# Kernel optimization log

Measured on AMD Instinct MI355X. Metric: run time of the kernel, lower is better.

The kernel has to match this reference:

```python
import jax, jax.numpy as jnp
import numpy as np

B, D_MODEL, HIDEEN, HEAD, IMG_H, IMG_W = 16, 512, 512, 8, 32, 32
D_K = D_MODEL // HEAD
EPS = 1e-5


def setup_inputs() -> dict:
    key = jax.random.key(0)
    ks = jax.random.split(key, 9)
    s_in = 1.0 / np.sqrt(D_MODEL)
    s_h = 1.0 / np.sqrt(HIDEEN)
    return {
        "x": jax.random.normal(ks[0], (B, D_MODEL, IMG_H, IMG_W), jnp.float32),
        "Wq": jax.random.uniform(ks[1], (HIDEEN, D_MODEL), jnp.float32, -s_in, s_in),
        "bq": jax.random.uniform(ks[2], (HIDEEN,), jnp.float32, -s_in, s_in),
        "Wk": jax.random.uniform(ks[3], (HIDEEN, D_MODEL), jnp.float32, -s_in, s_in),
        "bk": jax.random.uniform(ks[4], (HIDEEN,), jnp.float32, -s_in, s_in),
        "Wv": jax.random.uniform(ks[5], (HIDEEN, D_MODEL), jnp.float32, -s_in, s_in),
        "bv": jax.random.uniform(ks[6], (HIDEEN,), jnp.float32, -s_in, s_in),
        "Wo": jax.random.uniform(ks[7], (HIDEEN, HIDEEN), jnp.float32, -s_h, s_h),
        "bo": jax.random.uniform(ks[8], (HIDEEN,), jnp.float32, -s_h, s_h),
    }


def _conv1x1(x, W, b):
    # x: [B, Cin, H, W], W: [Cout, Cin]
    return jnp.einsum("bchw,oc->bohw", x, W) + b[None, :, None, None]


def _heads(t):
    # torch: [B, C, H, W] -> view(B, -1, head, d_k) -> transpose(1, 2)
    return t.reshape(B, -1, HEAD, D_K).transpose(0, 2, 1, 3)  # [B, head, N, d_k]


def reference(x, Wq, bq, Wk, bk, Wv, bv, Wo, bo):
    q = _heads(_conv1x1(x, Wq, bq))
    k = _heads(_conv1x1(x, Wk, bk))
    v = _heads(_conv1x1(x, Wv, bv))
    scores = jnp.einsum("bhnd,bhmd->bhnm", q, k) / np.sqrt(D_K).astype(np.float32)
    attn = jax.nn.softmax(scores, axis=-1)
    out = jnp.einsum("bhnm,bhmd->bhnd", attn, v)  # [B, head, N, d_k]
    # back to image layout: [B, N, head*d_k] -> [B, hideen, H, W]
    out = out.transpose(0, 2, 1, 3).reshape(B, -1, HEAD * D_K)
    out = out.transpose(0, 2, 1).reshape(B, -1, IMG_H, IMG_W)
    out = _conv1x1(out, Wo, bo)
    # InstanceNorm2d (affine=False, biased var, eps=1e-5)
    mu = out.mean(axis=(2, 3), keepdims=True)
    var = out.var(axis=(2, 3), keepdims=True)
    out = (out - mu) / jnp.sqrt(var + EPS)
    # original applies the SAME attn_out conv a second time
    out = _conv1x1(out, Wo, bo)
    return out
```

## Files before the change

### kernel.cpp

```cpp
#include <hip/hip_runtime.h>


typedef short bf16x8_t __attribute__((ext_vector_type(8)));
typedef float f32x4_t  __attribute__((ext_vector_type(4)));

union U4 { uint4 u; bf16x8_t v; unsigned short us[8]; };

__device__ __forceinline__ unsigned short f2bf(float f) {
  union { float f; unsigned int u; } x; x.f = f;
  unsigned int r = x.u + 0x7fffu + ((x.u >> 16) & 1u);
  return (unsigned short)(r >> 16);
}
__device__ __forceinline__ unsigned int f2bf2(float lo, float hi) {
  return (unsigned int)f2bf(lo) | ((unsigned int)f2bf(hi) << 16);
}
__device__ __forceinline__ void ld_lds16(const unsigned short* g,
                                         unsigned short* l) {
  __builtin_amdgcn_global_load_lds(
      (const __attribute__((address_space(1))) unsigned int*)g,
      (__attribute__((address_space(3))) unsigned int*)l, 16, 0, 0);
}

#define BATCH_STRIDE (512 * 1024)

__global__ __launch_bounds__(256) void cvtx_k(
    const float* __restrict__ x, unsigned short* __restrict__ xb)
{
  __shared__ float tile[32][33];
  const int b = blockIdx.z, c0 = blockIdx.y * 32, n0 = blockIdx.x * 32;
  const int t = threadIdx.x;
  {
    const int cr = t >> 3, n4 = (t & 7) * 4;
    const float4 u = *(const float4*)(x + (size_t)b * BATCH_STRIDE
                                      + (size_t)(c0 + cr) * 1024 + n0 + n4);
    tile[cr][n4] = u.x; tile[cr][n4 + 1] = u.y;
    tile[cr][n4 + 2] = u.z; tile[cr][n4 + 3] = u.w;
  }
  __syncthreads();
  {
    const int nl = t >> 3, c4 = (t & 7) * 4;
    uint2 o;
    o.x = f2bf2(tile[c4][nl], tile[c4 + 1][nl]);
    o.y = f2bf2(tile[c4 + 2][nl], tile[c4 + 3][nl]);
    *(uint2*)(xb + (size_t)b * BATCH_STRIDE + (size_t)(n0 + nl) * 512
              + c0 + c4) = o;
  }
}

template<int OUTF>
__device__ __forceinline__ void gemm_core(
    const float* __restrict__ W, const float* __restrict__ bias,
    const unsigned short* __restrict__ src, void* __restrict__ dst,
    int m0, int n0, int b, unsigned short* sA, unsigned short* sB)
{
  const int t = threadIdx.x;
  const int lane = t & 63, wv = t >> 6, qd = lane >> 4, cl = lane & 15;
  const int wm = wv >> 1, wn = wv & 1;
  const unsigned short* srcb = src + (size_t)b * BATCH_STRIDE + (size_t)n0 * 512;

  f32x4_t acc[4][4];
  #pragma unroll
  for (int i = 0; i < 4; ++i)
    #pragma unroll
    for (int f = 0; f < 4; ++f) acc[i][f] = (f32x4_t){0.f, 0.f, 0.f, 0.f};

  const int srow = t >> 2, sch = (t & 3) * 8;

  for (int kk = 0; kk < 512; kk += 32) {
    if (kk) __syncthreads();
    #pragma unroll
    for (int p = 0; p < 2; ++p) {
      ld_lds16(srcb + (size_t)(p * 64 + srow) * 512 + kk + sch,
               sB + p * 2048 + t * 8);
      const float* wr = W + (size_t)(m0 + p * 64 + srow) * 512 + kk + sch;
      const float4 w0 = *(const float4*)wr;
      const float4 w1 = *(const float4*)(wr + 4);
      uint4 wa;
      wa.x = f2bf2(w0.x, w0.y); wa.y = f2bf2(w0.z, w0.w);
      wa.z = f2bf2(w1.x, w1.y); wa.w = f2bf2(w1.z, w1.w);
      *(uint4*)(sA + p * 2048 + t * 8) = wa;
    }
    __syncthreads();
    U4 af[4], bfr[4];
    #pragma unroll
    for (int i = 0; i < 4; ++i) {
      af[i].u  = *(const uint4*)(sA + (wm * 64 + i * 16 + cl) * 32 + qd * 8);
      bfr[i].u = *(const uint4*)(sB + (wn * 64 + i * 16 + cl) * 32 + qd * 8);
    }
    #pragma unroll
    for (int i = 0; i < 4; ++i)
      #pragma unroll
      for (int f = 0; f < 4; ++f)
        acc[i][f] = __builtin_amdgcn_mfma_f32_16x16x32_bf16(
            af[i].v, bfr[f].v, acc[i][f], 0, 0, 0);
  }

  #pragma unroll
  for (int i = 0; i < 4; ++i) {
    #pragma unroll
    for (int r = 0; r < 4; ++r) {
      const int o = m0 + wm * 64 + i * 16 + qd * 4 + r;
      const float bv = bias[o];
      #pragma unroll
      for (int f = 0; f < 4; ++f) {
        const int n = n0 + wn * 64 + f * 16 + cl;
        const size_t idx = (size_t)b * BATCH_STRIDE + (size_t)o * 1024 + n;
        const float val = acc[i][f][r] + bv;
        if (OUTF) ((float*)dst)[idx] = val;
        else      ((unsigned short*)dst)[idx] = f2bf(val);
      }
    }
  }
}

struct QKVArgs {
  const float* W[3];
  const float* bias[3];
  unsigned short* dst[3];
};

__global__ __launch_bounds__(256) void qkv_k(
    QKVArgs args, const unsigned short* __restrict__ xb)
{
  __shared__ __align__(16) unsigned short sA[128 * 32];
  __shared__ __align__(16) unsigned short sB[128 * 32];
  const int widx = blockIdx.y >> 2;
  const int m0 = (blockIdx.y & 3) * 128;
  gemm_core<0>(args.W[widx], args.bias[widx], xb, args.dst[widx],
               m0, blockIdx.x * 128, blockIdx.z, sA, sB);
}

template<int OUTF>
__global__ __launch_bounds__(256) void gemm_wo_k(
    const float* __restrict__ W, const float* __restrict__ bias,
    const unsigned short* __restrict__ src, void* __restrict__ dst)
{
  __shared__ __align__(16) unsigned short sA[128 * 32];
  __shared__ __align__(16) unsigned short sB[128 * 32];
  gemm_core<OUTF>(W, bias, src, dst, blockIdx.y * 128, blockIdx.x * 128,
                  blockIdx.z, sA, sB);
}

__global__ __launch_bounds__(256) void vt_k(
    const unsigned short* __restrict__ V, unsigned short* __restrict__ Vt)
{
  __shared__ unsigned short sT[64 * 72];
  const int b = blockIdx.z, p0 = blockIdx.x * 64, j0 = blockIdx.y * 64;
  const int t = threadIdx.x;
  const int r = t >> 2, c8 = (t & 3) * 8;
  #pragma unroll
  for (int p = 0; p < 2; ++p)
    *(uint4*)(sT + r * 72 + c8 + p * 32) =
        *(const uint4*)(V + (size_t)b * BATCH_STRIDE
                        + (size_t)(p0 + r) * 512 + j0 + c8 + p * 32);
  __syncthreads();
  #pragma unroll
  for (int p = 0; p < 2; ++p) {
    U4 o;
    #pragma unroll
    for (int e = 0; e < 8; ++e) o.us[e] = sT[(c8 + p * 32 + e) * 72 + r];
    *(uint4*)(Vt + (size_t)b * BATCH_STRIDE + (size_t)(j0 + r) * 1024
              + p0 + c8 + p * 32) = o.u;
  }
}

__global__ __launch_bounds__(256) void attn_k(
    const unsigned short* __restrict__ Q,
    const unsigned short* __restrict__ K,
    const unsigned short* __restrict__ Vt,
    unsigned short* __restrict__ O)
{
  __shared__ __align__(16) unsigned short sK[64 * 80];
  __shared__ __align__(16) unsigned short sV[64 * 80];
  __shared__ __align__(16) unsigned short sP[4 * 32 * 80];

  const int t = threadIdx.x;
  const int lane = t & 63, wv = t >> 6, qd = lane >> 4, cl = lane & 15;
  const int b = blockIdx.y >> 3, h = blockIdx.y & 7;
  const int i0 = blockIdx.x * 128;
  const size_t bbase = (size_t)b * BATCH_STRIDE;
  const int hoff = h * 64;
  unsigned short* sPw = sP + wv * 2560;

  U4 aq[2][2];
  #pragma unroll
  for (int mt = 0; mt < 2; ++mt) {
    const unsigned short* qp =
        Q + bbase + (size_t)(i0 + wv * 32 + mt * 16 + cl) * 512 + hoff;
    aq[mt][0].u = *(const uint4*)(qp + qd * 8);
    aq[mt][1].u = *(const uint4*)(qp + 32 + qd * 8);
  }

  f32x4_t oacc[2][4];
  #pragma unroll
  for (int mt = 0; mt < 2; ++mt)
    #pragma unroll
    for (int f = 0; f < 4; ++f) oacc[mt][f] = (f32x4_t){0.f, 0.f, 0.f, 0.f};
  float rs[2][4] = {{0.f, 0.f, 0.f, 0.f}, {0.f, 0.f, 0.f, 0.f}};

  const int srow = t >> 2, sch = (t & 3) * 8;

  for (int j0 = 0; j0 < 1024; j0 += 64) {
    __syncthreads();
    #pragma unroll
    for (int p = 0; p < 2; ++p) {
      *(uint4*)(sK + srow * 80 + sch + p * 32) =
          *(const uint4*)(K + bbase + (size_t)(j0 + srow) * 512
                          + hoff + sch + p * 32);
      *(uint4*)(sV + srow * 80 + sch + p * 32) =
          *(const uint4*)(Vt + bbase + (size_t)(hoff + srow) * 1024
                          + j0 + sch + p * 32);
    }
    __syncthreads();

    f32x4_t s[2][4];
    #pragma unroll
    for (int nh = 0; nh < 4; ++nh) {
      U4 bk0, bk1;
      bk0.u = *(const uint4*)(sK + (nh * 16 + cl) * 80 + qd * 8);
      bk1.u = *(const uint4*)(sK + (nh * 16 + cl) * 80 + 32 + qd * 8);
      #pragma unroll
      for (int mt = 0; mt < 2; ++mt) {
        s[mt][nh] = (f32x4_t){0.f, 0.f, 0.f, 0.f};
        s[mt][nh] = __builtin_amdgcn_mfma_f32_16x16x32_bf16(
            aq[mt][0].v, bk0.v, s[mt][nh], 0, 0, 0);
        s[mt][nh] = __builtin_amdgcn_mfma_f32_16x16x32_bf16(
            aq[mt][1].v, bk1.v, s[mt][nh], 0, 0, 0);
      }
    }

    #pragma unroll
    for (int mt = 0; mt < 2; ++mt)
      #pragma unroll
      for (int nh = 0; nh < 4; ++nh)
        #pragma unroll
        for (int r = 0; r < 4; ++r) {
          const float pv = __expf(s[mt][nh][r] * 0.125f);
          sPw[(mt * 16 + qd * 4 + r) * 80 + nh * 16 + cl] = f2bf(pv);
          rs[mt][r] += pv;
        }

    __syncthreads();

    U4 pf[2][2];
    #pragma unroll
    for (int mt = 0; mt < 2; ++mt) {
      pf[mt][0].u = *(const uint4*)(sPw + (mt * 16 + cl) * 80 + qd * 8);
      pf[mt][1].u = *(const uint4*)(sPw + (mt * 16 + cl) * 80 + 32 + qd * 8);
    }
    #pragma unroll
    for (int f = 0; f < 4; ++f) {
      U4 vf0, vf1;
      vf0.u = *(const uint4*)(sV + (f * 16 + cl) * 80 + qd * 8);
      vf1.u = *(const uint4*)(sV + (f * 16 + cl) * 80 + 32 + qd * 8);
      #pragma unroll
      for (int mt = 0; mt < 2; ++mt) {
        oacc[mt][f] = __builtin_amdgcn_mfma_f32_16x16x32_bf16(
            pf[mt][0].v, vf0.v, oacc[mt][f], 0, 0, 0);
        oacc[mt][f] = __builtin_amdgcn_mfma_f32_16x16x32_bf16(
            pf[mt][1].v, vf1.v, oacc[mt][f], 0, 0, 0);
      }
    }
  }

  #pragma unroll
  for (int m = 1; m < 16; m <<= 1)
    #pragma unroll
    for (int mt = 0; mt < 2; ++mt)
      #pragma unroll
      for (int r = 0; r < 4; ++r) rs[mt][r] += __shfl_xor(rs[mt][r], m);

  #pragma unroll
  for (int mt = 0; mt < 2; ++mt)
    #pragma unroll
    for (int f = 0; f < 4; ++f)
      #pragma unroll
      for (int r = 0; r < 4; ++r) {
        const int i = i0 + wv * 32 + mt * 16 + qd * 4 + r;
        const int j = hoff + f * 16 + cl;
        O[bbase + (size_t)i * 512 + j] = f2bf(oacc[mt][f][r] / rs[mt][r]);
      }
}

__global__ __launch_bounds__(256) void norm_k(
    const float* __restrict__ x, unsigned short* __restrict__ y)
{
  __shared__ float tile[8][1028];
  __shared__ float shm[8], shv[8];
  const int b = blockIdx.x >> 6, c0 = (blockIdx.x & 63) * 8;
  const int t = threadIdx.x;
  const int ch = t >> 5, ln = t & 31;
  const float* xr = x + (size_t)b * BATCH_STRIDE + (size_t)(c0 + ch) * 1024;
  float s1 = 0.f, s2 = 0.f;
  #pragma unroll
  for (int j = 0; j < 8; ++j) {
    const int n = ln * 4 + j * 128;
    const float4 u = *(const float4*)(xr + n);
    tile[ch][n] = u.x; tile[ch][n + 1] = u.y;
    tile[ch][n + 2] = u.z; tile[ch][n + 3] = u.w;
    s1 += u.x + u.y + u.z + u.w;
    s2 += u.x * u.x + u.y * u.y + u.z * u.z + u.w * u.w;
  }
  #pragma unroll
  for (int m = 1; m < 32; m <<= 1) {
    s1 += __shfl_xor(s1, m);
    s2 += __shfl_xor(s2, m);
  }
  if (ln == 0) {
    const float mean = s1 * (1.f / 1024.f);
    const float var = s2 * (1.f / 1024.f) - mean * mean;
    shm[ch] = mean;
    shv[ch] = rsqrtf(var + 1e-5f);
  }
  __syncthreads();
  unsigned short* yb = y + (size_t)b * BATCH_STRIDE;
  #pragma unroll
  for (int jn = 0; jn < 4; ++jn) {
    const int n = t + jn * 256;
    uint4 o;
    o.x = f2bf2((tile[0][n] - shm[0]) * shv[0], (tile[1][n] - shm[1]) * shv[1]);
    o.y = f2bf2((tile[2][n] - shm[2]) * shv[2], (tile[3][n] - shm[3]) * shv[3]);
    o.z = f2bf2((tile[4][n] - shm[4]) * shv[4], (tile[5][n] - shm[5]) * shv[5]);
    o.w = f2bf2((tile[6][n] - shm[6]) * shv[6], (tile[7][n] - shm[7]) * shv[7]);
    *(uint4*)(yb + (size_t)n * 512 + c0) = o;
  }
}

extern "C" void kernel_launch(void* const* d_in, const int* in_sizes, int n_in,
                              void* d_out, int out_size, void* d_ws, size_t ws_size,
                              hipStream_t stream) {
  const float* x  = (const float*)d_in[0];
  const float* Wq = (const float*)d_in[1];
  const float* bq = (const float*)d_in[2];
  const float* Wk = (const float*)d_in[3];
  const float* bk = (const float*)d_in[4];
  const float* Wv = (const float*)d_in[5];
  const float* bv = (const float*)d_in[6];
  const float* Wo = (const float*)d_in[7];
  const float* bo = (const float*)d_in[8];

  const size_t BUF = (size_t)16 * BATCH_STRIDE;
  unsigned short* xb = (unsigned short*)d_ws;
  unsigned short* Qb = xb + BUF;
  unsigned short* Kb = Qb + BUF;
  unsigned short* Vb = (unsigned short*)d_out;
  unsigned short* Ob = Vb + BUF;
  unsigned short* Vt = xb;
  float*          out1f = (float*)d_ws;
  unsigned short* out1n = Kb;

  QKVArgs qa;
  qa.W[0] = Wq; qa.W[1] = Wk; qa.W[2] = Wv;
  qa.bias[0] = bq; qa.bias[1] = bk; qa.bias[2] = bv;
  qa.dst[0] = Qb; qa.dst[1] = Kb; qa.dst[2] = Vb;

  cvtx_k<<<dim3(32, 16, 16), 256, 0, stream>>>(x, xb);
  qkv_k<<<dim3(8, 12, 16), 256, 0, stream>>>(qa, xb);
  vt_k<<<dim3(16, 8, 16), 256, 0, stream>>>(Vb, Vt);
  attn_k<<<dim3(8, 128), 256, 0, stream>>>(Qb, Kb, Vt, Ob);
  gemm_wo_k<1><<<dim3(8, 4, 16), 256, 0, stream>>>(Wo, bo, Ob, out1f);
  norm_k<<<dim3(16 * 64), 256, 0, stream>>>(out1f, out1n);
  gemm_wo_k<1><<<dim3(8, 4, 16), 256, 0, stream>>>(Wo, bo, out1n, d_out);
}
```

Before: 298.2 us.

## Load attention K/V fragments directly from global, swizzle GEMM LDS, remap blocks per XCD

The attention kernel stops staging K and V tiles in shared memory and has each wave load its MFMA fragments straight from global memory into registers. This removes the block-wide barriers around the K/V tile. The per-wave P buffer shrinks to a 72-element stride and its block barrier becomes a compiler memory fence, since each wave only reads its own P. The launch becomes a flat 1D grid remapped so each XCD handles contiguous batch/head groups, aiming for better L2 locality. Separately, the shared GEMM core XOR-swizzles its LDS chunk layout to reduce bank conflicts. The risks are redundant global K/V reads across the four waves, higher register pressure, and relying on wave-synchronous LDS behaviour without a barrier.

After: 326.0 us. 1.09x slower.

```diff
diff --git a/kernel.cpp b/kernel.cpp
--- a/kernel.cpp
+++ b/kernel.cpp
@@ -64,15 +64,17 @@
     #pragma unroll
     for (int f = 0; f < 4; ++f) acc[i][f] = (f32x4_t){0.f, 0.f, 0.f, 0.f};
 
-  const int srow = t >> 2, sch = (t & 3) * 8;
+  const int srow = t >> 2;
+  const int cg = ((t & 3) ^ ((t >> 3) & 3)) * 8;
+  const int chunkoff = (qd ^ ((cl >> 1) & 3)) * 8;
 
   for (int kk = 0; kk < 512; kk += 32) {
     if (kk) __syncthreads();
     #pragma unroll
     for (int p = 0; p < 2; ++p) {
-      ld_lds16(srcb + (size_t)(p * 64 + srow) * 512 + kk + sch,
+      ld_lds16(srcb + (size_t)(p * 64 + srow) * 512 + kk + cg,
                sB + p * 2048 + t * 8);
-      const float* wr = W + (size_t)(m0 + p * 64 + srow) * 512 + kk + sch;
+      const float* wr = W + (size_t)(m0 + p * 64 + srow) * 512 + kk + cg;
       const float4 w0 = *(const float4*)wr;
       const float4 w1 = *(const float4*)(wr + 4);
       uint4 wa;
@@ -84,8 +86,8 @@
     U4 af[4], bfr[4];
     #pragma unroll
     for (int i = 0; i < 4; ++i) {
-      af[i].u  = *(const uint4*)(sA + (wm * 64 + i * 16 + cl) * 32 + qd * 8);
-      bfr[i].u = *(const uint4*)(sB + (wn * 64 + i * 16 + cl) * 32 + qd * 8);
+      af[i].u  = *(const uint4*)(sA + (wm * 64 + i * 16 + cl) * 32 + chunkoff);
+      bfr[i].u = *(const uint4*)(sB + (wn * 64 + i * 16 + cl) * 32 + chunkoff);
     }
     #pragma unroll
     for (int i = 0; i < 4; ++i)
@@ -170,17 +172,18 @@
     const unsigned short* __restrict__ Vt,
     unsigned short* __restrict__ O)
 {
-  __shared__ __align__(16) unsigned short sK[64 * 80];
-  __shared__ __align__(16) unsigned short sV[64 * 80];
-  __shared__ __align__(16) unsigned short sP[4 * 32 * 80];
+  __shared__ __align__(16) unsigned short sP[4 * 32 * 72];
 
   const int t = threadIdx.x;
   const int lane = t & 63, wv = t >> 6, qd = lane >> 4, cl = lane & 15;
-  const int b = blockIdx.y >> 3, h = blockIdx.y & 7;
-  const int i0 = blockIdx.x * 128;
+  const int id = blockIdx.x;
+  const int xcd = id & 7, y = id >> 3;
+  const int bh = xcd * 16 + (y & 15), it = y >> 4;
+  const int b = bh >> 3, h = bh & 7;
+  const int i0 = it * 128;
   const size_t bbase = (size_t)b * BATCH_STRIDE;
   const int hoff = h * 64;
-  unsigned short* sPw = sP + wv * 2560;
+  unsigned short* sPw = sP + wv * 2304;
 
   U4 aq[2][2];
   #pragma unroll
@@ -191,6 +194,9 @@
     aq[mt][1].u = *(const uint4*)(qp + 32 + qd * 8);
   }
 
+  const unsigned short* kb = K + bbase + (size_t)cl * 512 + hoff + qd * 8;
+  const unsigned short* vb = Vt + bbase + (size_t)(hoff + cl) * 1024 + qd * 8;
+
   f32x4_t oacc[2][4];
   #pragma unroll
   for (int mt = 0; mt < 2; ++mt)
@@ -198,36 +204,33 @@
     for (int f = 0; f < 4; ++f) oacc[mt][f] = (f32x4_t){0.f, 0.f, 0.f, 0.f};
   float rs[2][4] = {{0.f, 0.f, 0.f, 0.f}, {0.f, 0.f, 0.f, 0.f}};
 
-  const int srow = t >> 2, sch = (t & 3) * 8;
-
   for (int j0 = 0; j0 < 1024; j0 += 64) {
-    __syncthreads();
-    #pragma unroll
-    for (int p = 0; p < 2; ++p) {
-      *(uint4*)(sK + srow * 80 + sch + p * 32) =
-          *(const uint4*)(K + bbase + (size_t)(j0 + srow) * 512
-                          + hoff + sch + p * 32);
-      *(uint4*)(sV + srow * 80 + sch + p * 32) =
-          *(const uint4*)(Vt + bbase + (size_t)(hoff + srow) * 1024
-                          + j0 + sch + p * 32);
-    }
-    __syncthreads();
+    U4 kf[4][2];
+    #pragma unroll
+    for (int nh = 0; nh < 4; ++nh)
+      #pragma unroll
+      for (int hf = 0; hf < 2; ++hf)
+        kf[nh][hf].u = *(const uint4*)(kb + (size_t)(j0 + nh * 16) * 512
+                                       + hf * 32);
+    U4 vf[4][2];
+    #pragma unroll
+    for (int f = 0; f < 4; ++f)
+      #pragma unroll
+      for (int hf = 0; hf < 2; ++hf)
+        vf[f][hf].u = *(const uint4*)(vb + (size_t)(f * 16) * 1024
+                                      + j0 + hf * 32);
 
     f32x4_t s[2][4];
     #pragma unroll
-    for (int nh = 0; nh < 4; ++nh) {
-      U4 bk0, bk1;
-      bk0.u = *(const uint4*)(sK + (nh * 16 + cl) * 80 + qd * 8);
-      bk1.u = *(const uint4*)(sK + (nh * 16 + cl) * 80 + 32 + qd * 8);
+    for (int nh = 0; nh < 4; ++nh)
       #pragma unroll
       for (int mt = 0; mt < 2; ++mt) {
         s[mt][nh] = (f32x4_t){0.f, 0.f, 0.f, 0.f};
         s[mt][nh] = __builtin_amdgcn_mfma_f32_16x16x32_bf16(
-            aq[mt][0].v, bk0.v, s[mt][nh], 0, 0, 0);
+            aq[mt][0].v, kf[nh][0].v, s[mt][nh], 0, 0, 0);
         s[mt][nh] = __builtin_amdgcn_mfma_f32_16x16x32_bf16(
-            aq[mt][1].v, bk1.v, s[mt][nh], 0, 0, 0);
+            aq[mt][1].v, kf[nh][1].v, s[mt][nh], 0, 0, 0);
       }
-    }
 
     #pragma unroll
     for (int mt = 0; mt < 2; ++mt)
@@ -236,31 +239,27 @@
         #pragma unroll
         for (int r = 0; r < 4; ++r) {
           const float pv = __expf(s[mt][nh][r] * 0.125f);
-          sPw[(mt * 16 + qd * 4 + r) * 80 + nh * 16 + cl] = f2bf(pv);
+          sPw[(mt * 16 + qd * 4 + r) * 72 + nh * 16 + cl] = f2bf(pv);
           rs[mt][r] += pv;
         }
 
-    __syncthreads();
+    __asm__ __volatile__("" ::: "memory");
 
     U4 pf[2][2];
     #pragma unroll
     for (int mt = 0; mt < 2; ++mt) {
-      pf[mt][0].u = *(const uint4*)(sPw + (mt * 16 + cl) * 80 + qd * 8);
-      pf[mt][1].u = *(const uint4*)(sPw + (mt * 16 + cl) * 80 + 32 + qd * 8);
+      pf[mt][0].u = *(const uint4*)(sPw + (mt * 16 + cl) * 72 + qd * 8);
+      pf[mt][1].u = *(const uint4*)(sPw + (mt * 16 + cl) * 72 + 32 + qd * 8);
     }
     #pragma unroll
-    for (int f = 0; f < 4; ++f) {
-      U4 vf0, vf1;
-      vf0.u = *(const uint4*)(sV + (f * 16 + cl) * 80 + qd * 8);
-      vf1.u = *(const uint4*)(sV + (f * 16 + cl) * 80 + 32 + qd * 8);
+    for (int f = 0; f < 4; ++f)
       #pragma unroll
       for (int mt = 0; mt < 2; ++mt) {
         oacc[mt][f] = __builtin_amdgcn_mfma_f32_16x16x32_bf16(
-            pf[mt][0].v, vf0.v, oacc[mt][f], 0, 0, 0);
+            pf[mt][0].v, vf[f][0].v, oacc[mt][f], 0, 0, 0);
         oacc[mt][f] = __builtin_amdgcn_mfma_f32_16x16x32_bf16(
-            pf[mt][1].v, vf1.v, oacc[mt][f], 0, 0, 0);
+            pf[mt][1].v, vf[f][1].v, oacc[mt][f], 0, 0, 0);
       }
-    }
   }
 
   #pragma unroll
@@ -357,7 +356,7 @@
   cvtx_k<<<dim3(32, 16, 16), 256, 0, stream>>>(x, xb);
   qkv_k<<<dim3(8, 12, 16), 256, 0, stream>>>(qa, xb);
   vt_k<<<dim3(16, 8, 16), 256, 0, stream>>>(Vb, Vt);
-  attn_k<<<dim3(8, 128), 256, 0, stream>>>(Qb, Kb, Vt, Ob);
+  attn_k<<<dim3(1024), 256, 0, stream>>>(Qb, Kb, Vt, Ob);
   gemm_wo_k<1><<<dim3(8, 4, 16), 256, 0, stream>>>(Wo, bo, Ob, out1f);
   norm_k<<<dim3(16 * 64), 256, 0, stream>>>(out1f, out1n);
   gemm_wo_k<1><<<dim3(8, 4, 16), 256, 0, stream>>>(Wo, bo, out1n, d_out);
```

## Pre-convert weights to bf16, swizzle GEMM LDS, widen attention tiles with XCD mapping

Applied to the files above, without the earlier changes.

A new kernel converts Wq/Wk/Wv/Wo to bf16 once per call. The GEMM then streams both operands into LDS with async global_load_lds, using an XOR chunk swizzle to cut bank conflicts, instead of converting fp32 weights per tile. The attention kernel doubles the rows per block to 256 (64 per wave), so each K/V tile is reused across more queries. It computes exp right after each QK slice, and drops the block barrier around the per-wave P buffer, relying on a compiler fence. A 1D grid with XCD-aware block remapping groups each batch-head on one XCD for L2 locality. The costs are more VGPR pressure in attention, which may lower occupancy, one extra launch, and more scratch space in the workspace and output buffers.

After: 304.1 us. About the same (+2.0%).

```diff
diff --git a/kernel.cpp b/kernel.cpp
--- a/kernel.cpp
+++ b/kernel.cpp
@@ -47,9 +47,23 @@
   }
 }
 
+struct CvtWArgs { const float* src[4]; unsigned short* dst[4]; };
+
+__global__ __launch_bounds__(256) void cvtw_k(CvtWArgs a)
+{
+  const int m = blockIdx.y;
+  const int idx = blockIdx.x * 2048 + threadIdx.x * 8;
+  const float4 u0 = *(const float4*)(a.src[m] + idx);
+  const float4 u1 = *(const float4*)(a.src[m] + idx + 4);
+  uint4 o;
+  o.x = f2bf2(u0.x, u0.y); o.y = f2bf2(u0.z, u0.w);
+  o.z = f2bf2(u1.x, u1.y); o.w = f2bf2(u1.z, u1.w);
+  *(uint4*)(a.dst[m] + idx) = o;
+}
+
 template<int OUTF>
 __device__ __forceinline__ void gemm_core(
-    const float* __restrict__ W, const float* __restrict__ bias,
+    const unsigned short* __restrict__ Wb, const float* __restrict__ bias,
     const unsigned short* __restrict__ src, void* __restrict__ dst,
     int m0, int n0, int b, unsigned short* sA, unsigned short* sB)
 {
@@ -64,28 +78,25 @@
     #pragma unroll
     for (int f = 0; f < 4; ++f) acc[i][f] = (f32x4_t){0.f, 0.f, 0.f, 0.f};
 
-  const int srow = t >> 2, sch = (t & 3) * 8;
+  const int srow = t >> 2;
+  const int cg = ((t & 3) ^ ((t >> 3) & 3)) * 8;
+  const int chunkoff = (qd ^ ((cl >> 1) & 3)) * 8;
 
   for (int kk = 0; kk < 512; kk += 32) {
     if (kk) __syncthreads();
     #pragma unroll
     for (int p = 0; p < 2; ++p) {
-      ld_lds16(srcb + (size_t)(p * 64 + srow) * 512 + kk + sch,
+      ld_lds16(Wb + (size_t)(m0 + p * 64 + srow) * 512 + kk + cg,
+               sA + p * 2048 + t * 8);
+      ld_lds16(srcb + (size_t)(p * 64 + srow) * 512 + kk + cg,
                sB + p * 2048 + t * 8);
-      const float* wr = W + (size_t)(m0 + p * 64 + srow) * 512 + kk + sch;
-      const float4 w0 = *(const float4*)wr;
-      const float4 w1 = *(const float4*)(wr + 4);
-      uint4 wa;
-      wa.x = f2bf2(w0.x, w0.y); wa.y = f2bf2(w0.z, w0.w);
-      wa.z = f2bf2(w1.x, w1.y); wa.w = f2bf2(w1.z, w1.w);
-      *(uint4*)(sA + p * 2048 + t * 8) = wa;
     }
     __syncthreads();
     U4 af[4], bfr[4];
     #pragma unroll
     for (int i = 0; i < 4; ++i) {
-      af[i].u  = *(const uint4*)(sA + (wm * 64 + i * 16 + cl) * 32 + qd * 8);
-      bfr[i].u = *(const uint4*)(sB + (wn * 64 + i * 16 + cl) * 32 + qd * 8);
+      af[i].u  = *(const uint4*)(sA + (wm * 64 + i * 16 + cl) * 32 + chunkoff);
+      bfr[i].u = *(const uint4*)(sB + (wn * 64 + i * 16 + cl) * 32 + chunkoff);
     }
     #pragma unroll
     for (int i = 0; i < 4; ++i)
@@ -114,7 +125,7 @@
 }
 
 struct QKVArgs {
-  const float* W[3];
+  const unsigned short* W[3];
   const float* bias[3];
   unsigned short* dst[3];
 };
@@ -132,12 +143,12 @@
 
 template<int OUTF>
 __global__ __launch_bounds__(256) void gemm_wo_k(
-    const float* __restrict__ W, const float* __restrict__ bias,
+    const unsigned short* __restrict__ Wb, const float* __restrict__ bias,
     const unsigned short* __restrict__ src, void* __restrict__ dst)
 {
   __shared__ __align__(16) unsigned short sA[128 * 32];
   __shared__ __align__(16) unsigned short sB[128 * 32];
-  gemm_core<OUTF>(W, bias, src, dst, blockIdx.y * 128, blockIdx.x * 128,
+  gemm_core<OUTF>(Wb, bias, src, dst, blockIdx.y * 128, blockIdx.x * 128,
                   blockIdx.z, sA, sB);
 }
 
@@ -172,31 +183,38 @@
 {
   __shared__ __align__(16) unsigned short sK[64 * 80];
   __shared__ __align__(16) unsigned short sV[64 * 80];
-  __shared__ __align__(16) unsigned short sP[4 * 32 * 80];
+  __shared__ __align__(16) unsigned short sP[4 * 64 * 68];
 
   const int t = threadIdx.x;
   const int lane = t & 63, wv = t >> 6, qd = lane >> 4, cl = lane & 15;
-  const int b = blockIdx.y >> 3, h = blockIdx.y & 7;
-  const int i0 = blockIdx.x * 128;
+  const int id = blockIdx.x;
+  const int xcd = id & 7, s = id >> 3;
+  const int bh = xcd * 16 + (s & 15), it = s >> 4;
+  const int b = bh >> 3, h = bh & 7;
+  const int i0 = it * 256;
   const size_t bbase = (size_t)b * BATCH_STRIDE;
   const int hoff = h * 64;
-  unsigned short* sPw = sP + wv * 2560;
-
-  U4 aq[2][2];
-  #pragma unroll
-  for (int mt = 0; mt < 2; ++mt) {
+  unsigned short* sPw = sP + wv * (64 * 68);
+
+  U4 aq[4][2];
+  #pragma unroll
+  for (int mt = 0; mt < 4; ++mt) {
     const unsigned short* qp =
-        Q + bbase + (size_t)(i0 + wv * 32 + mt * 16 + cl) * 512 + hoff;
+        Q + bbase + (size_t)(i0 + wv * 64 + mt * 16 + cl) * 512 + hoff;
     aq[mt][0].u = *(const uint4*)(qp + qd * 8);
     aq[mt][1].u = *(const uint4*)(qp + 32 + qd * 8);
   }
 
-  f32x4_t oacc[2][4];
-  #pragma unroll
-  for (int mt = 0; mt < 2; ++mt)
+  f32x4_t oacc[4][4];
+  #pragma unroll
+  for (int mt = 0; mt < 4; ++mt)
     #pragma unroll
     for (int f = 0; f < 4; ++f) oacc[mt][f] = (f32x4_t){0.f, 0.f, 0.f, 0.f};
-  float rs[2][4] = {{0.f, 0.f, 0.f, 0.f}, {0.f, 0.f, 0.f, 0.f}};
+  float rs[4][4];
+  #pragma unroll
+  for (int mt = 0; mt < 4; ++mt)
+    #pragma unroll
+    for (int r = 0; r < 4; ++r) rs[mt][r] = 0.f;
 
   const int srow = t >> 2, sch = (t & 3) * 8;
 
@@ -213,40 +231,37 @@
     }
     __syncthreads();
 
-    f32x4_t s[2][4];
     #pragma unroll
     for (int nh = 0; nh < 4; ++nh) {
       U4 bk0, bk1;
       bk0.u = *(const uint4*)(sK + (nh * 16 + cl) * 80 + qd * 8);
       bk1.u = *(const uint4*)(sK + (nh * 16 + cl) * 80 + 32 + qd * 8);
-      #pragma unroll
-      for (int mt = 0; mt < 2; ++mt) {
-        s[mt][nh] = (f32x4_t){0.f, 0.f, 0.f, 0.f};
-        s[mt][nh] = __builtin_amdgcn_mfma_f32_16x16x32_bf16(
-            aq[mt][0].v, bk0.v, s[mt][nh], 0, 0, 0);
-        s[mt][nh] = __builtin_amdgcn_mfma_f32_16x16x32_bf16(
-            aq[mt][1].v, bk1.v, s[mt][nh], 0, 0, 0);
+      f32x4_t sreg[4];
+      #pragma unroll
+      for (int mt = 0; mt < 4; ++mt) {
+        sreg[mt] = (f32x4_t){0.f, 0.f, 0.f, 0.f};
+        sreg[mt] = __builtin_amdgcn_mfma_f32_16x16x32_bf16(
+            aq[mt][0].v, bk0.v, sreg[mt], 0, 0, 0);
+        sreg[mt] = __builtin_amdgcn_mfma_f32_16x16x32_bf16(
+            aq[mt][1].v, bk1.v, sreg[mt], 0, 0, 0);
       }
-    }
-
-    #pragma unroll
-    for (int mt = 0; mt < 2; ++mt)
-      #pragma unroll
-      for (int nh = 0; nh < 4; ++nh)
+      #pragma unroll
+      for (int mt = 0; mt < 4; ++mt)
         #pragma unroll
         for (int r = 0; r < 4; ++r) {
-          const float pv = __expf(s[mt][nh][r] * 0.125f);
-          sPw[(mt * 16 + qd * 4 + r) * 80 + nh * 16 + cl] = f2bf(pv);
+          const float pv = __expf(sreg[mt][r] * 0.125f);
+          sPw[(mt * 16 + qd * 4 + r) * 68 + nh * 16 + cl] = f2bf(pv);
           rs[mt][r] += pv;
         }
-
-    __syncthreads();
-
-    U4 pf[2][2];
-    #pragma unroll
-    for (int mt = 0; mt < 2; ++mt) {
-      pf[mt][0].u = *(const uint4*)(sPw + (mt * 16 + cl) * 80 + qd * 8);
-      pf[mt][1].u = *(const uint4*)(sPw + (mt * 16 + cl) * 80 + 32 + qd * 8);
+    }
+
+    __asm__ __volatile__("" ::: "memory");
+
+    U4 pf[4][2];
+    #pragma unroll
+    for (int mt = 0; mt < 4; ++mt) {
+      pf[mt][0].u = *(const uint4*)(sPw + (mt * 16 + cl) * 68 + qd * 8);
+      pf[mt][1].u = *(const uint4*)(sPw + (mt * 16 + cl) * 68 + 32 + qd * 8);
     }
     #pragma unroll
     for (int f = 0; f < 4; ++f) {
@@ -254,7 +269,7 @@
       vf0.u = *(const uint4*)(sV + (f * 16 + cl) * 80 + qd * 8);
       vf1.u = *(const uint4*)(sV + (f * 16 + cl) * 80 + 32 + qd * 8);
       #pragma unroll
-      for (int mt = 0; mt < 2; ++mt) {
+      for (int mt = 0; mt < 4; ++mt) {
         oacc[mt][f] = __builtin_amdgcn_mfma_f32_16x16x32_bf16(
             pf[mt][0].v, vf0.v, oacc[mt][f], 0, 0, 0);
         oacc[mt][f] = __builtin_amdgcn_mfma_f32_16x16x32_bf16(
@@ -266,17 +281,17 @@
   #pragma unroll
   for (int m = 1; m < 16; m <<= 1)
     #pragma unroll
-    for (int mt = 0; mt < 2; ++mt)
+    for (int mt = 0; mt < 4; ++mt)
       #pragma unroll
       for (int r = 0; r < 4; ++r) rs[mt][r] += __shfl_xor(rs[mt][r], m);
 
   #pragma unroll
-  for (int mt = 0; mt < 2; ++mt)
+  for (int mt = 0; mt < 4; ++mt)
     #pragma unroll
     for (int f = 0; f < 4; ++f)
       #pragma unroll
       for (int r = 0; r < 4; ++r) {
-        const int i = i0 + wv * 32 + mt * 16 + qd * 4 + r;
+        const int i = i0 + wv * 64 + mt * 16 + qd * 4 + r;
         const int j = hoff + f * 16 + cl;
         O[bbase + (size_t)i * 512 + j] = f2bf(oacc[mt][f][r] / rs[mt][r]);
       }
@@ -343,22 +358,32 @@
   unsigned short* xb = (unsigned short*)d_ws;
   unsigned short* Qb = xb + BUF;
   unsigned short* Kb = Qb + BUF;
-  unsigned short* Vb = (unsigned short*)d_out;
-  unsigned short* Ob = Vb + BUF;
+  unsigned short* WoB = Kb + BUF;
+  unsigned short* dscr = (unsigned short*)d_out;
+  unsigned short* Vb = dscr;
+  unsigned short* Ob = dscr + BUF;
+  unsigned short* WqB = dscr + BUF;
+  unsigned short* WkB = WqB + 262144;
+  unsigned short* WvB = WkB + 262144;
   unsigned short* Vt = xb;
   float*          out1f = (float*)d_ws;
   unsigned short* out1n = Kb;
 
+  CvtWArgs ca;
+  ca.src[0] = Wq; ca.src[1] = Wk; ca.src[2] = Wv; ca.src[3] = Wo;
+  ca.dst[0] = WqB; ca.dst[1] = WkB; ca.dst[2] = WvB; ca.dst[3] = WoB;
+
   QKVArgs qa;
-  qa.W[0] = Wq; qa.W[1] = Wk; qa.W[2] = Wv;
+  qa.W[0] = WqB; qa.W[1] = WkB; qa.W[2] = WvB;
   qa.bias[0] = bq; qa.bias[1] = bk; qa.bias[2] = bv;
   qa.dst[0] = Qb; qa.dst[1] = Kb; qa.dst[2] = Vb;
 
   cvtx_k<<<dim3(32, 16, 16), 256, 0, stream>>>(x, xb);
+  cvtw_k<<<dim3(128, 4), 256, 0, stream>>>(ca);
   qkv_k<<<dim3(8, 12, 16), 256, 0, stream>>>(qa, xb);
   vt_k<<<dim3(16, 8, 16), 256, 0, stream>>>(Vb, Vt);
-  attn_k<<<dim3(8, 128), 256, 0, stream>>>(Qb, Kb, Vt, Ob);
-  gemm_wo_k<1><<<dim3(8, 4, 16), 256, 0, stream>>>(Wo, bo, Ob, out1f);
+  attn_k<<<dim3(512), 256, 0, stream>>>(Qb, Kb, Vt, Ob);
+  gemm_wo_k<1><<<dim3(8, 4, 16), 256, 0, stream>>>(WoB, bo, Ob, out1f);
   norm_k<<<dim3(16 * 64), 256, 0, stream>>>(out1f, out1n);
-  gemm_wo_k<1><<<dim3(8, 4, 16), 256, 0, stream>>>(Wo, bo, out1n, d_out);
-}
+  gemm_wo_k<1><<<dim3(8, 4, 16), 256, 0, stream>>>(WoB, bo, out1n, d_out);
+}
```
